# Kernel optimization log

Measured on AMD Instinct MI355X. Metric: run time of the kernel, lower is better.

## Reference

```python
import jax, jax.numpy as jnp
import numpy as np

L, E, N, D, A = 3, 1000000, 100000, 64, 8
NREL = 230
NR2 = 2 * NREL + 1  # 461 relation embeddings
Q, ENT = 1000, 10000


def setup_inputs() -> dict:
    key = jax.random.key(0)
    ks = jax.random.split(key, 21)
    p = lambda k, shape: jax.random.normal(k, shape, dtype=jnp.float32) * 0.1
    return {
        "relation": jax.random.randint(ks[0], (Q,), 0, NR2, dtype=jnp.int32),
        "r_idx": jax.random.randint(ks[1], (L, E), 0, Q, dtype=jnp.int32),
        "rel": jax.random.randint(ks[2], (L, E), 0, NR2, dtype=jnp.int32),
        "sub": jax.random.randint(ks[3], (L, E), 0, N, dtype=jnp.int32),
        "obj": jax.random.randint(ks[4], (L, E), 0, N, dtype=jnp.int32),
        "idx": jnp.arange(N, dtype=jnp.int32),
        "nodes_q": jax.random.randint(ks[5], (N,), 0, Q, dtype=jnp.int32),
        "nodes_ent": jax.random.randint(ks[6], (N,), 0, ENT, dtype=jnp.int32),
        "rela_embed": p(ks[7], (L, NR2, D)),
        "Ws_w": p(ks[8], (L, A, D)),
        "Wr_w": p(ks[9], (L, A, D)),
        "Wqr_w": p(ks[10], (L, A, D)),
        "Wqr_b": p(ks[11], (L, A)),
        "walpha_w": p(ks[12], (L, 1, A)),
        "walpha_b": p(ks[13], (L, 1)),
        "Wh_w": p(ks[14], (L, D, D)),
        "gru_Wih": p(ks[15], (3 * D, D)),
        "gru_Whh": p(ks[16], (3 * D, D)),
        "gru_bih": p(ks[17], (3 * D,)),
        "gru_bhh": p(ks[18], (3 * D,)),
        "Wfinal_w": p(ks[19], (1, D)),
    }


def _gru_cell(x, h, Wih, Whh, bih, bhh):
    # torch nn.GRU single step: gates from input x and state h
    gi = x @ Wih.T + bih  # [N, 3D]
    gh = h @ Whh.T + bhh  # [N, 3D]
    i_r, i_z, i_n = jnp.split(gi, 3, axis=-1)
    h_r, h_z, h_n = jnp.split(gh, 3, axis=-1)
    r = jax.nn.sigmoid(i_r + h_r)
    z = jax.nn.sigmoid(i_z + h_z)
    n = jnp.tanh(i_n + r * h_n)
    return (1.0 - z) * n + z * h


def reference(relation, r_idx, rel, sub, obj, idx, nodes_q, nodes_ent,
              rela_embed, Ws_w, Wr_w, Wqr_w, Wqr_b, walpha_w, walpha_b, Wh_w,
              gru_Wih, gru_Whh, gru_bih, gru_bhh, Wfinal_w):
    hidden = jnp.zeros((N, D), dtype=jnp.float32)
    h0 = jnp.zeros((N, D), dtype=jnp.float32)
    for i in range(L):  # small fixed number of structurally distinct layers
        emb = rela_embed[i]
        hs = hidden[sub[i]]              # [E, D] gather of source node states
        hr = emb[rel[i]]                 # [E, D] relation embedding lookup
        h_qr = emb[relation[r_idx[i]]]   # [E, D] query-relation embedding
        attn = jax.nn.relu(hs @ Ws_w[i].T + hr @ Wr_w[i].T + h_qr @ Wqr_w[i].T + Wqr_b[i])
        alpha = jax.nn.sigmoid(attn @ walpha_w[i].T + walpha_b[i])  # [E, 1]
        message = alpha * (hs + hr)
        agg = jax.ops.segment_sum(message, obj[i], num_segments=N)  # scatter-add
        hidden = jax.nn.relu(agg @ Wh_w[i].T)
        # index_copy of previous state into new node ordering
        h0 = jnp.zeros((N, D), dtype=jnp.float32).at[idx].set(h0)
        h0 = _gru_cell(hidden, h0, gru_Wih, gru_Whh, gru_bih, gru_bhh)
        hidden = h0
    scores = (hidden @ Wfinal_w.T)[:, 0]  # [N]
    scores_all = jnp.zeros((Q, ENT), dtype=jnp.float32).at[nodes_q, nodes_ent].set(scores)
    return scores_all
```

## Files before the change

### kernel.cpp

```cpp
#include <hip/hip_runtime.h>
#include <math.h>

#define LL  3
#define EE  1000000
#define NNODE 100000
#define DD  64
#define AAT 8
#define NR2C 461
#define QQ  1000
#define ENTC 10000
#define QE  (QQ * ENTC)

#define NB    782
#define NWGL  128
#define CHUNK 7813
#define CAPB  4096

#define PS_LDS (CHUNK * 8 + NB * 4 * 2 + 256 * 4)

#define SCAN_N (NB * NWGL)
#define SCAN_TILE 4096
#define SCAN_TILES ((SCAN_N + SCAN_TILE - 1) / SCAN_TILE)

#define NTILES (NNODE / 16)
#define NWTILES 58
#define FRAG_U4_PER_LAYER (NWTILES * 2 * 64)

typedef __attribute__((ext_vector_type(8))) short s8v;
typedef __attribute__((ext_vector_type(4))) float f4v;

__device__ __forceinline__ float sigmoidf_(float x) {
    return 1.0f / (1.0f + __expf(-x));
}
__device__ __forceinline__ float tanhf_(float x) {
    return 1.0f - 2.0f / (__expf(2.0f * x) + 1.0f);
}
__device__ __forceinline__ unsigned short bf16rne(float f) {
    unsigned u = __float_as_uint(f);
    return (unsigned short)((u + 0x7FFFu + ((u >> 16) & 1u)) >> 16);
}
__device__ __forceinline__ float bf16tof(unsigned short b) {
    return __uint_as_float(((unsigned)b) << 16);
}

__device__ __forceinline__ float dot8_reduce(float* p, int lane) {
#pragma unroll
    for (int st = 1; st < 8; st <<= 1)
#pragma unroll
        for (int a = 0; a < 8; ++a)
            p[a] += __shfl_xor(p[a], st, 64);
    const int aid = lane & 7;
    float v = p[0];
#pragma unroll
    for (int j = 1; j < 8; ++j)
        v = (aid == j) ? p[j] : v;
    v += __shfl_xor(v, 8, 64);
    v += __shfl_xor(v, 16, 64);
    v += __shfl_xor(v, 32, 64);
    return v;
}

__global__ void fill_f32(float* __restrict__ p, int n, float v) {
    int i = blockIdx.x * blockDim.x + threadIdx.x;
    int stride = gridDim.x * blockDim.x;
    float4* p4 = (float4*)p;
    int n4 = n >> 2;
    float4 v4 = make_float4(v, v, v, v);
    for (int j = i; j < n4; j += stride) p4[j] = v4;
}

__global__ void fill_i32(int* __restrict__ p, int n, int v) {
    int i = blockIdx.x * blockDim.x + threadIdx.x;
    int stride = gridDim.x * blockDim.x;
    int4* p4 = (int4*)p;
    int n4 = n >> 2;
    int4 v4 = make_int4(v, v, v, v);
    for (int j = i; j < n4; j += stride) p4[j] = v4;
}


__global__ __launch_bounds__(256) void part_hist(
    const int* __restrict__ obj, int* __restrict__ hist)
{
    const int l = blockIdx.y, wg = blockIdx.x;
    const int* o = obj + l * EE;
    __shared__ int cnt[NB];
    for (int b = threadIdx.x; b < NB; b += 256) cnt[b] = 0;
    __syncthreads();
    const int s = wg * CHUNK;
    const int e = (s + CHUNK < EE) ? s + CHUNK : EE;
    for (int p = s + threadIdx.x; p < e; p += 256)
        atomicAdd(&cnt[o[p] >> 7], 1);
    __syncthreads();
    int* hh = hist + l * (NB * NWGL);
    for (int b = threadIdx.x; b < NB; b += 256)
        hh[b * NWGL + wg] = cnt[b];
}

__global__ __launch_bounds__(1024) void scan_tiles_reduce(
    const int* __restrict__ hist, int* __restrict__ totals)
{
    const int l = blockIdx.y, tile = blockIdx.x;
    const int* hh = hist + l * SCAN_N;
    const int idx = tile * SCAN_TILE + threadIdx.x * 4;
    int s = 0;
    if (idx < SCAN_N) {
        const int4 v = *(const int4*)(hh + idx);
        s = v.x + v.y + v.z + v.w;
    }
#pragma unroll
    for (int st = 1; st < 64; st <<= 1) s += __shfl_xor(s, st, 64);
    __shared__ int ws[16];
    if ((threadIdx.x & 63) == 0) ws[threadIdx.x >> 6] = s;
    __syncthreads();
    if (threadIdx.x == 0) {
        int t = 0;
#pragma unroll
        for (int i = 0; i < 16; ++i) t += ws[i];
        totals[l * SCAN_TILES + tile] = t;
    }
}

__global__ __launch_bounds__(1024) void scan_tiles_scan(
    int* __restrict__ hist, const int* __restrict__ totals,
    int* __restrict__ bucketptr)
{
    const int l = blockIdx.y, tile = blockIdx.x;
    int* hh = hist + l * SCAN_N;
    int* bp = bucketptr + l * (NB + 1);
    const int t = threadIdx.x;
    __shared__ int lds[1024];
    __shared__ int toff_s;
    if (t < 64) {
        int o = (t < tile) ? totals[l * SCAN_TILES + t] : 0;
#pragma unroll
        for (int st = 1; st < 64; st <<= 1) o += __shfl_xor(o, st, 64);
        if (t == 0) toff_s = o;
    }
    const int idx = tile * SCAN_TILE + t * 4;
    int4 v = make_int4(0, 0, 0, 0);
    if (idx < SCAN_N) v = *(const int4*)(hh + idx);
    const int tsum = v.x + v.y + v.z + v.w;
    lds[t] = tsum;
    __syncthreads();
    for (int st = 1; st < 1024; st <<= 1) {
        const int u = (t >= st) ? lds[t - st] : 0;
        __syncthreads();
        lds[t] += u;
        __syncthreads();
    }
    const int excl = lds[t] - tsum + toff_s;
    if (idx < SCAN_N) {
        int4 o;
        o.x = excl;
        o.y = excl + v.x;
        o.z = o.y + v.y;
        o.w = o.z + v.z;
        *(int4*)(hh + idx) = o;
        if ((idx & 127) == 0) bp[idx >> 7] = o.x;
    }
    if (t == 0 && tile == 0) bp[NB] = EE;
}

__global__ __launch_bounds__(256) void part_scatter(
    const int* __restrict__ obj, const int* __restrict__ sub,
    const int* __restrict__ rel, const int* __restrict__ r_idx,
    const int* __restrict__ hist, unsigned long long* __restrict__ pk64)
{
    extern __shared__ unsigned long long stg[];
    int* cnt   = (int*)(stg + CHUNK);
    int* delta = cnt + NB;
    int* psum  = delta + NB;
    const int l = blockIdx.y, wg = blockIdx.x;
    const int* o  = obj + l * EE;
    const int* ss = sub + l * EE;
    const int* rr = rel + l * EE;
    const int* qq = r_idx + l * EE;
    unsigned long long* pk = pk64 + (size_t)l * EE;
    const int* hh = hist + l * (NB * NWGL);
    const int t = threadIdx.x;
    const int s0 = wg * CHUNK;
    const int e0 = (s0 + CHUNK < EE) ? s0 + CHUNK : EE;
    const int ne = e0 - s0;

    for (int b = t; b < NB; b += 256) cnt[b] = 0;
    __syncthreads();
    for (int p = s0 + t; p < e0; p += 256)
        atomicAdd(&cnt[o[p] >> 7], 1);
    __syncthreads();

    {
        const int b0 = t * 4;
        int local[4];
        int s = 0;
#pragma unroll
        for (int j = 0; j < 4; ++j) {
            const int idx = b0 + j;
            local[j] = (idx < NB) ? cnt[idx] : 0;
            s += local[j];
        }
        psum[t] = s;
        __syncthreads();
        for (int st = 1; st < 256; st <<= 1) {
            const int v = (t >= st) ? psum[t - st] : 0;
            __syncthreads();
            psum[t] += v;
            __syncthreads();
        }
        int run = (t == 0) ? 0 : psum[t - 1];
#pragma unroll
        for (int j = 0; j < 4; ++j) {
            const int idx = b0 + j;
            if (idx < NB) {
                cnt[idx] = run;
                delta[idx] = hh[idx * NWGL + wg] - run;
                run += local[j];
            }
        }
    }
    __syncthreads();

    for (int p = s0 + t; p < e0; p += 256) {
        const int ov = o[p];
        const int b = ov >> 7;
        const int k = atomicAdd(&cnt[b], 1);
        stg[k] = (unsigned long long)(unsigned)ss[p]
               | ((unsigned long long)(unsigned)rr[p] << 17)
               | ((unsigned long long)(unsigned)qq[p] << 26)
               | ((unsigned long long)(unsigned)(ov & 127) << 36)
               | ((unsigned long long)(unsigned)b << 43);
    }
    __syncthreads();

    for (int i = t; i < ne; i += 256) {
        const unsigned long long u = stg[i];
        const int b = (int)((u >> 43) & 0x3FF);
        pk[delta[b] + i] = u;
    }
}

__global__ __launch_bounds__(256) void bucket_sort(
    const int* __restrict__ bucketptr, unsigned long long* __restrict__ pk64,
    int* __restrict__ rowptr)
{
    const int l = blockIdx.y, b = blockIdx.x;
    unsigned long long* pk = pk64 + (size_t)l * EE;
    const int* bp = bucketptr + l * (NB + 1);
    const int base = bp[b], endp = bp[b + 1];
    const int ne = endp - base;
    extern __shared__ unsigned long long stg[];
    unsigned long long* srt = stg + CAPB;
    __shared__ int cnt[128];
    __shared__ int off[128];
    const int t = threadIdx.x;
    if (t < 128) cnt[t] = 0;
    __syncthreads();
    for (int i = t; i < ne; i += 256) {
        const unsigned long long u = pk[base + i];
        stg[i] = u;
        atomicAdd(&cnt[(int)((u >> 36) & 127)], 1);
    }
    __syncthreads();
    if (t == 0) {
        int run = 0;
#pragma unroll 8
        for (int o2 = 0; o2 < 128; ++o2) { off[o2] = run; run += cnt[o2]; }
    }
    __syncthreads();
    if (t < 128) {
        const int node = b * 128 + t;
        if (node < NNODE) rowptr[l * NNODE + node] = base + off[t] + cnt[t];
    }
    __syncthreads();
    for (int i = t; i < ne; i += 256) {
        const unsigned long long u = stg[i];
        const int pos = atomicAdd(&off[(int)((u >> 36) & 127)], 1);
        srt[pos] = u;
    }
    __syncthreads();
    for (int i = t; i < ne; i += 256)
        pk[base + i] = srt[i];
}


__global__ __launch_bounds__(256) void rqatt_kernel(
    const int* __restrict__ relation, const float* __restrict__ emb,
    const float* __restrict__ Wr, const float* __restrict__ Wqr,
    const float* __restrict__ Wqrb,
    float* __restrict__ r_att, float* __restrict__ qr_att)
{
    const int lane = threadIdx.x & 63;
    const int wid = (blockIdx.x * blockDim.x + threadIdx.x) >> 6;
    const int nw = (gridDim.x * blockDim.x) >> 6;
    float wr8[8], wq8[8];
#pragma unroll
    for (int a = 0; a < 8; ++a) {
        wr8[a] = Wr[a * 64 + lane];
        wq8[a] = Wqr[a * 64 + lane];
    }
    for (int i = wid; i < NR2C + QQ; i += nw) {
        const bool isQ = i >= NR2C;
        const int row = isQ ? relation[i - NR2C] : i;
        const float ev = emb[row * 64 + lane];
        float p[8];
#pragma unroll
        for (int a = 0; a < 8; ++a) p[a] = ev * (isQ ? wq8[a] : wr8[a]);
        float v = dot8_reduce(p, lane);
        if (lane < 8) {
            if (isQ) qr_att[(i - NR2C) * 8 + lane] = v + Wqrb[lane];
            else     r_att[i * 8 + lane] = v;
        }
    }
}

template<bool L0>
__global__ __launch_bounds__(256) void alpha_csr(
    const unsigned long long* __restrict__ pk64,
    const float* __restrict__ s_att, const float* __restrict__ r_att,
    const float* __restrict__ qr_att,
    const float* __restrict__ walw, const float* __restrict__ walb,
    float* __restrict__ alpha_p)
{
    const int e = blockIdx.x * blockDim.x + threadIdx.x;
    if (e >= EE) return;
    const unsigned long long u = pk64[e];
    const int s = (int)(u & 0x1FFFF);
    const int r = (int)((u >> 17) & 0x1FF);
    const int q = (int)((u >> 26) & 0x3FF);
    const float4* ra = (const float4*)(r_att + r * 8);
    const float4* qa = (const float4*)(qr_att + q * 8);
    const float4 r0 = ra[0], r1 = ra[1];
    const float4 q0 = qa[0], q1 = qa[1];
    float v0 = r0.x + q0.x, v1 = r0.y + q0.y, v2 = r0.z + q0.z, v3 = r0.w + q0.w;
    float v4 = r1.x + q1.x, v5 = r1.y + q1.y, v6 = r1.z + q1.z, v7 = r1.w + q1.w;
    if (!L0) {
        const float4* sa = (const float4*)(s_att + s * 8);
        const float4 s0 = sa[0], s1 = sa[1];
        v0 += s0.x; v1 += s0.y; v2 += s0.z; v3 += s0.w;
        v4 += s1.x; v5 += s1.y; v6 += s1.z; v7 += s1.w;
    }
    float t = walb[0];
    t += walw[0] * fmaxf(v0, 0.0f);
    t += walw[1] * fmaxf(v1, 0.0f);
    t += walw[2] * fmaxf(v2, 0.0f);
    t += walw[3] * fmaxf(v3, 0.0f);
    t += walw[4] * fmaxf(v4, 0.0f);
    t += walw[5] * fmaxf(v5, 0.0f);
    t += walw[6] * fmaxf(v6, 0.0f);
    t += walw[7] * fmaxf(v7, 0.0f);
    alpha_p[e] = sigmoidf_(t);
}

template<bool L0>
__device__ __forceinline__ float gather_term(
    const unsigned long long* __restrict__ pk64,
    const float* __restrict__ alpha_p, int p,
    const float* __restrict__ h, const float* __restrict__ emb, int lane)
{
    const unsigned long long u = pk64[p];
    const float a = alpha_p[p];
    const int s = (int)(u & 0x1FFFF);
    const int r = (int)((u >> 17) & 0x1FF);
    float m = emb[r * 64 + lane];
    if (!L0) m += h[s * 64 + lane];
    return a * m;
}

template<bool L0>
__global__ __launch_bounds__(256) void agg_gather(
    const int* __restrict__ rowptr, const unsigned long long* __restrict__ pk64,
    const float* __restrict__ alpha_p,
    const float* __restrict__ h, const float* __restrict__ emb,
    float* __restrict__ agg)
{
    const int lane = threadIdx.x & 63;
    const int wid = (blockIdx.x * blockDim.x + threadIdx.x) >> 6;
    const int nw = (gridDim.x * blockDim.x) >> 6;
    for (int n = wid; n < NNODE; n += nw) {
        const int start = __builtin_amdgcn_readfirstlane((n == 0) ? 0 : rowptr[n - 1]);
        const int end   = __builtin_amdgcn_readfirstlane(rowptr[n]);
        float a0 = 0.0f, a1 = 0.0f, a2 = 0.0f, a3 = 0.0f;
        int p = start;
        for (; p + 3 < end; p += 4) {
            a0 += gather_term<L0>(pk64, alpha_p, p,     h, emb, lane);
            a1 += gather_term<L0>(pk64, alpha_p, p + 1, h, emb, lane);
            a2 += gather_term<L0>(pk64, alpha_p, p + 2, h, emb, lane);
            a3 += gather_term<L0>(pk64, alpha_p, p + 3, h, emb, lane);
        }
        for (; p < end; ++p)
            a0 += gather_term<L0>(pk64, alpha_p, p, h, emb, lane);
        agg[n * 64 + lane] = (a0 + a1) + (a2 + a3);
    }
}


__global__ __launch_bounds__(128) void build_frags(
    const float* __restrict__ Wh_all, const float* __restrict__ Wih,
    const float* __restrict__ Whh, const float* __restrict__ Ws_all,
    uint4* __restrict__ frag)
{
    const int li = blockIdx.y;
    const int tile = blockIdx.x;
    const int term = threadIdx.x >> 6;
    const int lane_s = threadIdx.x & 63;
    const int rs = lane_s & 15, gs = lane_s >> 4;
    const float* Wh = Wh_all + li * DD * DD;
    const float* WsNext = Ws_all + (li + 1) * AAT * DD;
    unsigned short pk[8];
#pragma unroll
    for (int i = 0; i < 8; ++i) {
        const int kl = 16 * (i >> 2) + 4 * gs + (i & 3);
        float f;
        if (tile < 8)       { const int mt = tile >> 1, kf = tile & 1;
                              f = Wh[(mt * 16 + rs) * 64 + kf * 32 + kl]; }
        else if (tile < 40) { const int t2 = tile - 8, mt = t2 >> 2, kf = t2 & 3;
                              const int j = mt * 16 + rs, k = kf * 32 + kl;
                              f = (k < 64) ? Wih[j * 64 + k] : Whh[j * 64 + k - 64]; }
        else if (tile < 48) { const int t2 = tile - 40, mt = t2 >> 1, kf = t2 & 1;
                              f = Wih[(128 + mt * 16 + rs) * 64 + kf * 32 + kl]; }
        else if (tile < 56) { const int t2 = tile - 48, mt = t2 >> 1, kf = t2 & 1;
                              f = Whh[(128 + mt * 16 + rs) * 64 + kf * 32 + kl]; }
        else                { const int kf = tile - 56;
                              f = (li < 2 && rs < 8) ? WsNext[rs * 64 + kf * 32 + kl] : 0.0f; }
        if (term == 0) pk[i] = bf16rne(f);
        else { const float hi = bf16tof(bf16rne(f)); pk[i] = bf16rne(f - hi); }
    }
    uint4 w;
    w.x = (unsigned)pk[0] | ((unsigned)pk[1] << 16);
    w.y = (unsigned)pk[2] | ((unsigned)pk[3] << 16);
    w.z = (unsigned)pk[4] | ((unsigned)pk[5] << 16);
    w.w = (unsigned)pk[6] | ((unsigned)pk[7] << 16);
    frag[((size_t)li * NWTILES + tile) * 128 + term * 64 + lane_s] = w;
}

__device__ __forceinline__ void make_bfrag(const float* d16, s8v* hi, s8v* lo) {
#pragma unroll
    for (int t = 0; t < 2; ++t) {
        s8v hv, lv;
#pragma unroll
        for (int i = 0; i < 8; ++i) {
            const float f = d16[(2 * t + (i >> 2)) * 4 + (i & 3)];
            const unsigned short hb = bf16rne(f);
            hv[i] = (short)hb;
            lv[i] = (short)bf16rne(f - bf16tof(hb));
        }
        hi[t] = hv; lo[t] = lv;
    }
}

__device__ __forceinline__ f4v mm3(const s8v* __restrict__ afr, int tile, int lane,
                                   s8v bh, s8v bl, f4v c) {
    const s8v ah = afr[(tile * 2 + 0) * 64 + lane];
    const s8v al = afr[(tile * 2 + 1) * 64 + lane];
    c = __builtin_amdgcn_mfma_f32_16x16x32_bf16(ah, bh, c, 0, 0, 0);
    c = __builtin_amdgcn_mfma_f32_16x16x32_bf16(ah, bl, c, 0, 0, 0);
    c = __builtin_amdgcn_mfma_f32_16x16x32_bf16(al, bh, c, 0, 0, 0);
    return c;
}

__device__ __forceinline__ void ld16(const float* p, float* d) {
#pragma unroll
    for (int mt = 0; mt < 4; ++mt) {
        const float4 v = *(const float4*)(p + 16 * mt);
        d[mt * 4 + 0] = v.x; d[mt * 4 + 1] = v.y;
        d[mt * 4 + 2] = v.z; d[mt * 4 + 3] = v.w;
    }
}

template<bool L0, bool SATT, bool SCORE>
__global__ __launch_bounds__(256, 4) void node_mfma(
    const uint4* __restrict__ frag,
    const float* __restrict__ bih, const float* __restrict__ bhh,
    const float* __restrict__ Wf,
    float* __restrict__ h, const float* __restrict__ agg,
    float* __restrict__ s_att, float* __restrict__ scores)
{
    const int tid = threadIdx.x;
    const int lane = tid & 63;
    const int wslot = (blockIdx.x * 256 + tid) >> 6;
    const int base = wslot * 16;
    if (base >= NNODE) return;
    const int r = lane & 15, g = lane >> 4;
    const s8v* afr = (const s8v*)frag;

    float ag[16], hp[16];
    ld16(agg + (base + r) * 64 + 4 * g, ag);
    if (!L0) ld16(h + (base + r) * 64 + 4 * g, hp);
    else {
#pragma unroll
        for (int i = 0; i < 16; ++i) hp[i] = 0.0f;
    }
    s8v agh[2], agl[2];
    make_bfrag(ag, agh, agl);
    s8v hh2[2], hl2[2];
    if (!L0) make_bfrag(hp, hh2, hl2);

    float xd[16];
#pragma unroll
    for (int mt = 0; mt < 4; ++mt) {
        f4v acc = {0.0f, 0.0f, 0.0f, 0.0f};
        acc = mm3(afr, mt * 2 + 0, lane, agh[0], agl[0], acc);
        acc = mm3(afr, mt * 2 + 1, lane, agh[1], agl[1], acc);
#pragma unroll
        for (int c = 0; c < 4; ++c) xd[mt * 4 + c] = fmaxf(acc[c], 0.0f);
    }
    s8v xh[2], xl[2];
    make_bfrag(xd, xh, xl);

    f4v rz[8];
#pragma unroll
    for (int mt = 0; mt < 4; ++mt) {
        const int j0 = 16 * mt + 4 * g;
        const float4 a = *(const float4*)(bih + j0);
        const float4 b = *(const float4*)(bhh + j0);
        f4v t; t[0] = a.x + b.x; t[1] = a.y + b.y; t[2] = a.z + b.z; t[3] = a.w + b.w;
        rz[mt] = t;
        const float4 a2 = *(const float4*)(bih + 64 + j0);
        const float4 b2 = *(const float4*)(bhh + 64 + j0);
        f4v t2; t2[0] = a2.x + b2.x; t2[1] = a2.y + b2.y; t2[2] = a2.z + b2.z; t2[3] = a2.w + b2.w;
        rz[mt + 4] = t2;
    }
#pragma unroll
    for (int mt = 0; mt < 8; ++mt) {
        f4v acc = rz[mt];
        acc = mm3(afr, 8 + mt * 4 + 0, lane, xh[0], xl[0], acc);
        acc = mm3(afr, 8 + mt * 4 + 1, lane, xh[1], xl[1], acc);
        if (!L0) {
            acc = mm3(afr, 8 + mt * 4 + 2, lane, hh2[0], hl2[0], acc);
            acc = mm3(afr, 8 + mt * 4 + 3, lane, hh2[1], hl2[1], acc);
        }
        rz[mt] = acc;
    }

    f4v in4[4], hn4[4];
#pragma unroll
    for (int mt = 0; mt < 4; ++mt) {
        const int j0 = 16 * mt + 4 * g;
        const float4 a = *(const float4*)(bih + 128 + j0);
        f4v t; t[0] = a.x; t[1] = a.y; t[2] = a.z; t[3] = a.w;
        in4[mt] = t;
        const float4 b = *(const float4*)(bhh + 128 + j0);
        f4v t2; t2[0] = b.x; t2[1] = b.y; t2[2] = b.z; t2[3] = b.w;
        hn4[mt] = t2;
    }
#pragma unroll
    for (int mt = 0; mt < 4; ++mt) {
        f4v acc = in4[mt];
        acc = mm3(afr, 40 + mt * 2 + 0, lane, xh[0], xl[0], acc);
        acc = mm3(afr, 40 + mt * 2 + 1, lane, xh[1], xl[1], acc);
        in4[mt] = acc;
        if (!L0) {
            f4v a2 = hn4[mt];
            a2 = mm3(afr, 48 + mt * 2 + 0, lane, hh2[0], hl2[0], a2);
            a2 = mm3(afr, 48 + mt * 2 + 1, lane, hh2[1], hl2[1], a2);
            hn4[mt] = a2;
        }
    }

    float ho[16];
#pragma unroll
    for (int mt = 0; mt < 4; ++mt)
#pragma unroll
        for (int c = 0; c < 4; ++c) {
            const float rr = sigmoidf_(rz[mt][c]);
            const float zz = sigmoidf_(rz[mt + 4][c]);
            const float nn = tanhf_(in4[mt][c] + rr * hn4[mt][c]);
            ho[mt * 4 + c] = (1.0f - zz) * nn + zz * hp[mt * 4 + c];
        }

    if (!SCORE) {
        float* hop = h + (base + r) * 64 + 4 * g;
#pragma unroll
        for (int mt = 0; mt < 4; ++mt)
            *(float4*)(hop + 16 * mt) = make_float4(ho[mt * 4 + 0], ho[mt * 4 + 1],
                                                    ho[mt * 4 + 2], ho[mt * 4 + 3]);
    }
    if (SATT) {
        s8v oh[2], ol[2];
        make_bfrag(ho, oh, ol);
        f4v sa = {0.0f, 0.0f, 0.0f, 0.0f};
        sa = mm3(afr, 56, lane, oh[0], ol[0], sa);
        sa = mm3(afr, 57, lane, oh[1], ol[1], sa);
        if (g < 2) {
#pragma unroll
            for (int c = 0; c < 4; ++c)
                s_att[(base + r) * 8 + 4 * g + c] = sa[c];
        }
    }
    if (SCORE) {
        float s = 0.0f;
        const float* wfp = Wf + 4 * g;
#pragma unroll
        for (int mt = 0; mt < 4; ++mt) {
            const float4 w = *(const float4*)(wfp + 16 * mt);
            s += ho[mt * 4 + 0] * w.x + ho[mt * 4 + 1] * w.y
               + ho[mt * 4 + 2] * w.z + ho[mt * 4 + 3] * w.w;
        }
        s += __shfl_xor(s, 16, 64);
        s += __shfl_xor(s, 32, 64);
        if (lane < 16) scores[base + r] = s;
    }
}

__global__ void scatter_max_kernel(const int* __restrict__ nq, const int* __restrict__ ne,
                                   int* __restrict__ winner)
{
    int n = blockIdx.x * blockDim.x + threadIdx.x;
    if (n < NNODE) {
        int pos = nq[n] * ENTC + ne[n];
        atomicMax(&winner[pos], n);
    }
}

__global__ void scatter_write_kernel(const int* __restrict__ nq, const int* __restrict__ ne,
                                     const int* __restrict__ winner,
                                     const float* __restrict__ scores,
                                     float* __restrict__ out)
{
    int n = blockIdx.x * blockDim.x + threadIdx.x;
    if (n < NNODE) {
        int pos = nq[n] * ENTC + ne[n];
        if (winner[pos] == n) out[pos] = scores[n];
    }
}

extern "C" void kernel_launch(void* const* d_in, const int* in_sizes, int n_in,
                              void* d_out, int out_size, void* d_ws, size_t ws_size,
                              hipStream_t stream)
{
    const int* relation  = (const int*)d_in[0];
    const int* r_idx     = (const int*)d_in[1];
    const int* rel       = (const int*)d_in[2];
    const int* sub       = (const int*)d_in[3];
    const int* obj       = (const int*)d_in[4];
    const int* nodes_q   = (const int*)d_in[6];
    const int* nodes_ent = (const int*)d_in[7];
    const float* rela    = (const float*)d_in[8];
    const float* Ws      = (const float*)d_in[9];
    const float* Wr      = (const float*)d_in[10];
    const float* Wqr     = (const float*)d_in[11];
    const float* Wqrb    = (const float*)d_in[12];
    const float* walw    = (const float*)d_in[13];
    const float* walb    = (const float*)d_in[14];
    const float* Wh      = (const float*)d_in[15];
    const float* gWih    = (const float*)d_in[16];
    const float* gWhh    = (const float*)d_in[17];
    const float* gbih    = (const float*)d_in[18];
    const float* gbhh    = (const float*)d_in[19];
    const float* Wf      = (const float*)d_in[20];

    float* ws     = (float*)d_ws;
    float* scores = ws;
    float* h      = ws + 102400;
    float* agg    = h + NNODE * DD;
    int*   winner = (int*)(ws + 102400);
    float* out    = (float*)d_out;

    unsigned long long* pk64 = (unsigned long long*)d_out;
    uint4* fragbuf  = (uint4*)((float*)d_out + 6000000);
    float* s_att    = (float*)d_out + 6000000 + 3 * FRAG_U4_PER_LAYER * 4;
    float* r_att    = s_att + NNODE * 8;
    float* qr_att   = r_att + NR2C * 8;
    int*   rowptr   = (int*)(qr_att + QQ * 8);
    int*   hist     = rowptr + 3 * NNODE;
    int*   bucketpt = hist + 3 * NB * NWGL;
    int*   totals   = bucketpt + 3 * (NB + 1);
    float* alpha_p  = (float*)(totals + 3 * SCAN_TILES);

    part_hist<<<dim3(NWGL, 3), 256, 0, stream>>>(obj, hist);
    scan_tiles_reduce<<<dim3(SCAN_TILES, 3), 1024, 0, stream>>>(hist, totals);
    scan_tiles_scan<<<dim3(SCAN_TILES, 3), 1024, 0, stream>>>(hist, totals, bucketpt);
    part_scatter<<<dim3(NWGL, 3), 256, PS_LDS, stream>>>(obj, sub, rel, r_idx, hist, pk64);
    bucket_sort<<<dim3(NB, 3), 256, CAPB * 16, stream>>>(bucketpt, pk64, rowptr);
    build_frags<<<dim3(NWTILES, 3), 128, 0, stream>>>(Wh, gWih, gWhh, Ws, fragbuf);

    const int NODE_GRID = (NTILES * 64 + 255) / 256;
    for (int i = 0; i < LL; ++i) {
        const float* emb = rela + i * NR2C * DD;
        const uint4* fr = fragbuf + (size_t)i * FRAG_U4_PER_LAYER;
        rqatt_kernel<<<184, 256, 0, stream>>>(relation, emb,
            Wr + i * AAT * DD, Wqr + i * AAT * DD, Wqrb + i * AAT, r_att, qr_att);
        if (i == 0) {
            alpha_csr<true><<<(EE + 255) / 256, 256, 0, stream>>>(
                pk64, s_att, r_att, qr_att, walw, walb, alpha_p);
            agg_gather<true><<<2048, 256, 0, stream>>>(
                rowptr, pk64, alpha_p, h, emb, agg);
            node_mfma<true, true, false><<<NODE_GRID, 256, 0, stream>>>(
                fr, gbih, gbhh, Wf, h, agg, s_att, scores);
        } else {
            alpha_csr<false><<<(EE + 255) / 256, 256, 0, stream>>>(
                pk64 + (size_t)i * EE, s_att, r_att, qr_att,
                walw + i * AAT, walb + i, alpha_p);
            agg_gather<false><<<2048, 256, 0, stream>>>(
                rowptr + i * NNODE, pk64 + (size_t)i * EE, alpha_p, h, emb, agg);
            if (i == 1)
                node_mfma<false, true, false><<<NODE_GRID, 256, 0, stream>>>(
                    fr, gbih, gbhh, Wf, h, agg, s_att, scores);
            else
                node_mfma<false, false, true><<<NODE_GRID, 256, 0, stream>>>(
                    fr, gbih, gbhh, Wf, h, agg, s_att, scores);
        }
    }

    fill_f32<<<2048, 256, 0, stream>>>(out, QE, 0.0f);
    fill_i32<<<2048, 256, 0, stream>>>(winner, QE, -1);
    scatter_max_kernel<<<(NNODE + 255) / 256, 256, 0, stream>>>(nodes_q, nodes_ent, winner);
    scatter_write_kernel<<<(NNODE + 255) / 256, 256, 0, stream>>>(nodes_q, nodes_ent, winner, scores, out);
}
```

Before: 579.9 us.

## Replace per-node CSR sort with per-bucket LDS atomic aggregation

Drops the bucket_sort pass and the rowptr array. Aggregation now runs one block per 128-node bucket, accumulating edge messages into a 128x64 shared-memory tile with LDS float atomics before writing it out. The partition kernels now use 256 workgroups with smaller chunks, and the two output fill kernels are merged into one. This removes a full read/write pass over the packed edges, at the cost of LDS atomic contention, nondeterministic summation order, and fewer, coarser aggregation blocks.

After: 1.690 ms. 191% more time.

```diff
diff --git a/kernel.cpp b/kernel.cpp
--- a/kernel.cpp
+++ b/kernel.cpp
@@ -12,10 +12,8 @@
 #define QE  (QQ * ENTC)
 
 #define NB    782
-#define NWGL  128
-#define CHUNK 7813
-#define CAPB  4096
-
+#define NWGL  256
+#define CHUNK 3907
 #define PS_LDS (CHUNK * 8 + NB * 4 * 2 + 256 * 4)
 
 #define SCAN_N (NB * NWGL)
@@ -60,22 +58,14 @@
     return v;
 }
 
-__global__ void fill_f32(float* __restrict__ p, int n, float v) {
+__global__ void fill_final(float* __restrict__ out, int* __restrict__ winner) {
     int i = blockIdx.x * blockDim.x + threadIdx.x;
     int stride = gridDim.x * blockDim.x;
-    float4* p4 = (float4*)p;
-    int n4 = n >> 2;
-    float4 v4 = make_float4(v, v, v, v);
-    for (int j = i; j < n4; j += stride) p4[j] = v4;
-}
-
-__global__ void fill_i32(int* __restrict__ p, int n, int v) {
-    int i = blockIdx.x * blockDim.x + threadIdx.x;
-    int stride = gridDim.x * blockDim.x;
-    int4* p4 = (int4*)p;
-    int n4 = n >> 2;
-    int4 v4 = make_int4(v, v, v, v);
-    for (int j = i; j < n4; j += stride) p4[j] = v4;
+    float4* o4 = (float4*)out;
+    int4* w4 = (int4*)winner;
+    const float4 z = make_float4(0.f, 0.f, 0.f, 0.f);
+    const int4 m = make_int4(-1, -1, -1, -1);
+    for (int j = i; j < QE / 4; j += stride) { o4[j] = z; w4[j] = m; }
 }
 
 
@@ -157,7 +147,7 @@
         o.z = o.y + v.y;
         o.w = o.z + v.z;
         *(int4*)(hh + idx) = o;
-        if ((idx & 127) == 0) bp[idx >> 7] = o.x;
+        if ((idx & (NWGL - 1)) == 0) bp[idx / NWGL] = o.x;
     }
     if (t == 0 && tile == 0) bp[NB] = EE;
 }
@@ -237,49 +227,6 @@
         const int b = (int)((u >> 43) & 0x3FF);
         pk[delta[b] + i] = u;
     }
-}
-
-__global__ __launch_bounds__(256) void bucket_sort(
-    const int* __restrict__ bucketptr, unsigned long long* __restrict__ pk64,
-    int* __restrict__ rowptr)
-{
-    const int l = blockIdx.y, b = blockIdx.x;
-    unsigned long long* pk = pk64 + (size_t)l * EE;
-    const int* bp = bucketptr + l * (NB + 1);
-    const int base = bp[b], endp = bp[b + 1];
-    const int ne = endp - base;
-    extern __shared__ unsigned long long stg[];
-    unsigned long long* srt = stg + CAPB;
-    __shared__ int cnt[128];
-    __shared__ int off[128];
-    const int t = threadIdx.x;
-    if (t < 128) cnt[t] = 0;
-    __syncthreads();
-    for (int i = t; i < ne; i += 256) {
-        const unsigned long long u = pk[base + i];
-        stg[i] = u;
-        atomicAdd(&cnt[(int)((u >> 36) & 127)], 1);
-    }
-    __syncthreads();
-    if (t == 0) {
-        int run = 0;
-#pragma unroll 8
-        for (int o2 = 0; o2 < 128; ++o2) { off[o2] = run; run += cnt[o2]; }
-    }
-    __syncthreads();
-    if (t < 128) {
-        const int node = b * 128 + t;
-        if (node < NNODE) rowptr[l * NNODE + node] = base + off[t] + cnt[t];
-    }
-    __syncthreads();
-    for (int i = t; i < ne; i += 256) {
-        const unsigned long long u = stg[i];
-        const int pos = atomicAdd(&off[(int)((u >> 36) & 127)], 1);
-        srt[pos] = u;
-    }
-    __syncthreads();
-    for (int i = t; i < ne; i += 256)
-        pk[base + i] = srt[i];
 }
 
 
@@ -352,45 +299,58 @@
 }
 
 template<bool L0>
-__device__ __forceinline__ float gather_term(
-    const unsigned long long* __restrict__ pk64,
-    const float* __restrict__ alpha_p, int p,
-    const float* __restrict__ h, const float* __restrict__ emb, int lane)
-{
-    const unsigned long long u = pk64[p];
-    const float a = alpha_p[p];
-    const int s = (int)(u & 0x1FFFF);
-    const int r = (int)((u >> 17) & 0x1FF);
-    float m = emb[r * 64 + lane];
-    if (!L0) m += h[s * 64 + lane];
-    return a * m;
-}
-
-template<bool L0>
-__global__ __launch_bounds__(256) void agg_gather(
-    const int* __restrict__ rowptr, const unsigned long long* __restrict__ pk64,
+__global__ __launch_bounds__(256, 4) void agg_bucket(
+    const int* __restrict__ bucketptr, const unsigned long long* __restrict__ pk64,
     const float* __restrict__ alpha_p,
     const float* __restrict__ h, const float* __restrict__ emb,
     float* __restrict__ agg)
 {
-    const int lane = threadIdx.x & 63;
-    const int wid = (blockIdx.x * blockDim.x + threadIdx.x) >> 6;
-    const int nw = (gridDim.x * blockDim.x) >> 6;
-    for (int n = wid; n < NNODE; n += nw) {
-        const int start = __builtin_amdgcn_readfirstlane((n == 0) ? 0 : rowptr[n - 1]);
-        const int end   = __builtin_amdgcn_readfirstlane(rowptr[n]);
-        float a0 = 0.0f, a1 = 0.0f, a2 = 0.0f, a3 = 0.0f;
-        int p = start;
-        for (; p + 3 < end; p += 4) {
-            a0 += gather_term<L0>(pk64, alpha_p, p,     h, emb, lane);
-            a1 += gather_term<L0>(pk64, alpha_p, p + 1, h, emb, lane);
-            a2 += gather_term<L0>(pk64, alpha_p, p + 2, h, emb, lane);
-            a3 += gather_term<L0>(pk64, alpha_p, p + 3, h, emb, lane);
-        }
-        for (; p < end; ++p)
-            a0 += gather_term<L0>(pk64, alpha_p, p, h, emb, lane);
-        agg[n * 64 + lane] = (a0 + a1) + (a2 + a3);
-    }
+    __shared__ float acc[128 * 64];
+    const int b = blockIdx.x;
+    const int t = threadIdx.x;
+    const int lane = t & 63;
+    const int wv = t >> 6;
+    float4* a4 = (float4*)acc;
+    for (int i = t; i < 128 * 16; i += 256)
+        a4[i] = make_float4(0.f, 0.f, 0.f, 0.f);
+    __syncthreads();
+    const int start = __builtin_amdgcn_readfirstlane(bucketptr[b]);
+    const int end   = __builtin_amdgcn_readfirstlane(bucketptr[b + 1]);
+    int p0 = start + wv * 2;
+    for (; p0 + 1 < end; p0 += 8) {
+        const int pa = __builtin_amdgcn_readfirstlane(p0);
+        const unsigned long long u0 = pk64[pa];
+        const unsigned long long u1 = pk64[pa + 1];
+        const float al0 = alpha_p[pa];
+        const float al1 = alpha_p[pa + 1];
+        const int s0 = (int)(u0 & 0x1FFFF), r0 = (int)((u0 >> 17) & 0x1FF);
+        const int o0 = (int)((u0 >> 36) & 127);
+        const int s1 = (int)(u1 & 0x1FFFF), r1 = (int)((u1 >> 17) & 0x1FF);
+        const int o1 = (int)((u1 >> 36) & 127);
+        float m0 = emb[r0 * 64 + lane];
+        float m1 = emb[r1 * 64 + lane];
+        if (!L0) {
+            m0 += h[s0 * 64 + lane];
+            m1 += h[s1 * 64 + lane];
+        }
+        atomicAdd(&acc[o0 * 64 + lane], al0 * m0);
+        atomicAdd(&acc[o1 * 64 + lane], al1 * m1);
+    }
+    if (p0 < end) {
+        const int pa = __builtin_amdgcn_readfirstlane(p0);
+        const unsigned long long u0 = pk64[pa];
+        const float al0 = alpha_p[pa];
+        const int s0 = (int)(u0 & 0x1FFFF), r0 = (int)((u0 >> 17) & 0x1FF);
+        const int o0 = (int)((u0 >> 36) & 127);
+        float m0 = emb[r0 * 64 + lane];
+        if (!L0) m0 += h[s0 * 64 + lane];
+        atomicAdd(&acc[o0 * 64 + lane], al0 * m0);
+    }
+    __syncthreads();
+    const int nrow = (NNODE - b * 128 < 128) ? (NNODE - b * 128) : 128;
+    float* ao = agg + (size_t)b * 128 * 64;
+    for (int i = t; i < nrow * 64; i += 256)
+        ao[i] = acc[i];
 }
 
 
@@ -661,8 +621,7 @@
     float* s_att    = (float*)d_out + 6000000 + 3 * FRAG_U4_PER_LAYER * 4;
     float* r_att    = s_att + NNODE * 8;
     float* qr_att   = r_att + NR2C * 8;
-    int*   rowptr   = (int*)(qr_att + QQ * 8);
-    int*   hist     = rowptr + 3 * NNODE;
+    int*   hist     = (int*)(qr_att + QQ * 8);
     int*   bucketpt = hist + 3 * NB * NWGL;
     int*   totals   = bucketpt + 3 * (NB + 1);
     float* alpha_p  = (float*)(totals + 3 * SCAN_TILES);
@@ -671,7 +630,6 @@
     scan_tiles_reduce<<<dim3(SCAN_TILES, 3), 1024, 0, stream>>>(hist, totals);
     scan_tiles_scan<<<dim3(SCAN_TILES, 3), 1024, 0, stream>>>(hist, totals, bucketpt);
     part_scatter<<<dim3(NWGL, 3), 256, PS_LDS, stream>>>(obj, sub, rel, r_idx, hist, pk64);
-    bucket_sort<<<dim3(NB, 3), 256, CAPB * 16, stream>>>(bucketpt, pk64, rowptr);
     build_frags<<<dim3(NWTILES, 3), 128, 0, stream>>>(Wh, gWih, gWhh, Ws, fragbuf);
 
     const int NODE_GRID = (NTILES * 64 + 255) / 256;
@@ -683,16 +641,16 @@
         if (i == 0) {
             alpha_csr<true><<<(EE + 255) / 256, 256, 0, stream>>>(
                 pk64, s_att, r_att, qr_att, walw, walb, alpha_p);
-            agg_gather<true><<<2048, 256, 0, stream>>>(
-                rowptr, pk64, alpha_p, h, emb, agg);
+            agg_bucket<true><<<NB, 256, 0, stream>>>(
+                bucketpt, pk64, alpha_p, h, emb, agg);
             node_mfma<true, true, false><<<NODE_GRID, 256, 0, stream>>>(
                 fr, gbih, gbhh, Wf, h, agg, s_att, scores);
         } else {
             alpha_csr<false><<<(EE + 255) / 256, 256, 0, stream>>>(
                 pk64 + (size_t)i * EE, s_att, r_att, qr_att,
                 walw + i * AAT, walb + i, alpha_p);
-            agg_gather<false><<<2048, 256, 0, stream>>>(
-                rowptr + i * NNODE, pk64 + (size_t)i * EE, alpha_p, h, emb, agg);
+            agg_bucket<false><<<NB, 256, 0, stream>>>(
+                bucketpt + i * (NB + 1), pk64 + (size_t)i * EE, alpha_p, h, emb, agg);
             if (i == 1)
                 node_mfma<false, true, false><<<NODE_GRID, 256, 0, stream>>>(
                     fr, gbih, gbhh, Wf, h, agg, s_att, scores);
@@ -702,8 +660,7 @@
         }
     }
 
-    fill_f32<<<2048, 256, 0, stream>>>(out, QE, 0.0f);
-    fill_i32<<<2048, 256, 0, stream>>>(winner, QE, -1);
+    fill_final<<<2048, 256, 0, stream>>>(out, winner);
     scatter_max_kernel<<<(NNODE + 255) / 256, 256, 0, stream>>>(nodes_q, nodes_ent, winner);
     scatter_write_kernel<<<(NNODE + 255) / 256, 256, 0, stream>>>(nodes_q, nodes_ent, winner, scores, out);
 }
```
